# Performance work log

Measured on AMD Instinct MI355X. Metric: run time of the kernel, lower is better.

Reference implementation:

```python
import jax, jax.numpy as jnp
import numpy as np

N_NODES = 50000
N_EDGES = 640000
IN_CH = 64
EDGE_DIM = 16
HID = 128
OUT = 128
L = 5
N_GRAPHS = 128
BN_EPS = 1e-5


def setup_inputs() -> dict:
    key = jax.random.key(0)
    ks = jax.random.split(key, 16)

    def w(k, shape, fan_in):
        return jax.random.normal(k, shape, jnp.float32) / np.sqrt(fan_in)

    inp = {}
    inp["x"] = jax.random.normal(ks[0], (N_NODES, IN_CH), jnp.float32)
    inp["edge_index"] = jax.random.randint(ks[1], (2, N_EDGES), 0, N_NODES)
    inp["edge_attr"] = jax.random.normal(ks[2], (N_EDGES, EDGE_DIM), jnp.float32)
    inp["batch"] = jnp.sort(jax.random.randint(ks[3], (N_NODES,), 0, N_GRAPHS))
    # node / edge encoders
    inp["node_w"] = w(ks[4], (IN_CH, HID), IN_CH)
    inp["node_b"] = jnp.zeros((HID,), jnp.float32)
    inp["edge_w"] = w(ks[5], (EDGE_DIM, HID), EDGE_DIM)
    inp["edge_b"] = jnp.zeros((HID,), jnp.float32)
    # per-layer GINEConv params (stacked over L layers)
    inp["eps"] = jnp.zeros((L,), jnp.float32)  # train_eps init 0
    inp["lin_w"] = w(ks[6], (L, HID, HID), HID)       # GINEConv internal edge lin
    inp["lin_b"] = jnp.zeros((L, HID), jnp.float32)
    inp["mlp1_w"] = w(ks[7], (L, HID, 2 * HID), HID)
    inp["mlp1_b"] = jnp.zeros((L, 2 * HID), jnp.float32)
    inp["mlp2_w"] = w(ks[8], (L, 2 * HID, HID), 2 * HID)
    inp["mlp2_b"] = jnp.zeros((L, HID), jnp.float32)
    inp["bn_g"] = jnp.ones((L, HID), jnp.float32)
    inp["bn_b"] = jnp.zeros((L, HID), jnp.float32)
    # output MLP: HID -> HID//2 -> OUT
    inp["out_w1"] = w(ks[9], (HID, HID // 2), HID)
    inp["out_b1"] = jnp.zeros((HID // 2,), jnp.float32)
    inp["out_w2"] = w(ks[10], (HID // 2, OUT), HID // 2)
    inp["out_b2"] = jnp.zeros((OUT,), jnp.float32)
    return inp


def reference(x, edge_index, edge_attr, batch, node_w, node_b, edge_w, edge_b,
              eps, lin_w, lin_b, mlp1_w, mlp1_b, mlp2_w, mlp2_b, bn_g, bn_b,
              out_w1, out_b1, out_w2, out_b2):
    n_nodes = x.shape[0]
    src, dst = edge_index[0], edge_index[1]
    # node / edge encoders (dropout is identity in eval)
    h = jax.nn.relu(x @ node_w + node_b)            # [N, H]
    e = edge_attr @ edge_w + edge_b                  # [E, H]
    n_layers = lin_w.shape[0]
    for l in range(n_layers):
        # GINEConv: message = relu(x_src + lin(edge_emb)); aggregate = scatter-sum to dst
        m = jax.nn.relu(h[src] + e @ lin_w[l] + lin_b[l])      # [E, H]
        agg = jax.ops.segment_sum(m, dst, num_segments=n_nodes)  # [N, H]
        z = (1.0 + eps[l]) * h + agg
        # GINE MLP: H -> 2H -> H
        z = jax.nn.relu(z @ mlp1_w[l] + mlp1_b[l]) @ mlp2_w[l] + mlp2_b[l]
        # BatchNorm over nodes (training-mode batch statistics)
        mu = z.mean(axis=0)
        var = z.var(axis=0)
        z = (z - mu) * jax.lax.rsqrt(var + BN_EPS) * bn_g[l] + bn_b[l]
        # residual then relu
        h = jax.nn.relu(z + h)
    # global mean pool per graph
    counts = jax.ops.segment_sum(jnp.ones((n_nodes,), h.dtype), batch, num_segments=N_GRAPHS)
    pooled = jax.ops.segment_sum(h, batch, num_segments=N_GRAPHS) / jnp.maximum(counts, 1.0)[:, None]
    # output MLP (dropout identity in eval)
    logits = jax.nn.relu(pooled @ out_w1 + out_b1) @ out_w2 + out_b2
    return (logits, pooled)
```

## Files before the change

### kernel.cpp

```cpp
#include <hip/hip_runtime.h>

#define N_NODES  50000
#define NPAD     50048
#define N_EDGES  640000
#define IN_CH    64
#define EDGE_DIM 16
#define HID      128
#define HID2     256
#define NLAYER   5
#define NGRAPH   128
#define MT64     (NPAD / 64)

typedef unsigned short ushort_t;
typedef __attribute__((ext_vector_type(8))) short short8;
typedef __attribute__((ext_vector_type(4))) short s16x4;
typedef __attribute__((ext_vector_type(4))) float f32x4;
typedef __attribute__((ext_vector_type(2))) float f32x2;

__device__ __forceinline__ float b2f(ushort_t u) {
    union { unsigned v; float f; } x; x.v = ((unsigned)u) << 16; return x.f;
}
__device__ __forceinline__ ushort_t f2b(float f) {
    union { float f; unsigned u; } x; x.f = f;
    unsigned u = x.u;
    unsigned r = (u + 0x7FFFu + ((u >> 16) & 1u)) >> 16;
    return (ushort_t)r;
}

__global__ void k_transpose_cvt(const float* __restrict__ src, ushort_t* __restrict__ dst,
                                int B, int K, int Nn) {
    long total = (long)B * K * Nn;
    for (long i = (long)blockIdx.x * blockDim.x + threadIdx.x; i < total;
         i += (long)gridDim.x * blockDim.x) {
        int b = (int)(i / ((long)K * Nn));
        int rem = (int)(i - (long)b * K * Nn);
        int k = rem / Nn;
        int n = rem - k * Nn;
        dst[(long)b * K * Nn + (long)n * K + k] = f2b(src[i]);
    }
}

__global__ __launch_bounds__(128) void k_combine(const float* __restrict__ ew,
                                                 const float* __restrict__ eb,
                                                 const float* __restrict__ lw,
                                                 const float* __restrict__ lb,
                                                 ushort_t* __restrict__ WcbT,
                                                 float* __restrict__ cc) {
    int l = blockIdx.x, j = threadIdx.x;
    float accW[EDGE_DIM];
#pragma unroll
    for (int k = 0; k < EDGE_DIM; ++k) accW[k] = 0.f;
    float accc = 0.f;
    for (int i = 0; i < HID; ++i) {
        float lwv = lw[((long)l * HID + i) * HID + j];
        accc = fmaf(eb[i], lwv, accc);
#pragma unroll
        for (int k = 0; k < EDGE_DIM; ++k)
            accW[k] = fmaf(ew[k * HID + i], lwv, accW[k]);
    }
    ushort_t* wp = WcbT + ((long)l * HID + j) * 32;
#pragma unroll
    for (int k = 0; k < EDGE_DIM; ++k) wp[k] = f2b(accW[k]);
#pragma unroll
    for (int k = EDGE_DIM; k < 32; ++k) wp[k] = 0;
    cc[l * HID + j] = accc + lb[l * HID + j];
}

__global__ __launch_bounds__(256) void k_hist(const int* __restrict__ ei, int* __restrict__ deg) {
    int e = blockIdx.x * 256 + threadIdx.x;
    if (e < N_EDGES) atomicAdd(&deg[ei[N_EDGES + e]], 1);
}

__global__ __launch_bounds__(1024) void k_scan1(const int* __restrict__ deg,
                                                int* __restrict__ offs, int* __restrict__ bsum) {
    __shared__ int s[1024];
    int i = blockIdx.x * 1024 + threadIdx.x;
    int v = (i < N_NODES) ? deg[i] : 0;
    s[threadIdx.x] = v;
    __syncthreads();
    for (int off = 1; off < 1024; off <<= 1) {
        int t = (threadIdx.x >= off) ? s[threadIdx.x - off] : 0;
        __syncthreads();
        s[threadIdx.x] += t;
        __syncthreads();
    }
    if (i < N_NODES) offs[i] = s[threadIdx.x] - v;
    if (threadIdx.x == 1023) bsum[blockIdx.x] = s[1023];
}

__global__ void k_scan2(int* __restrict__ bsum, int nb) {
    if (threadIdx.x == 0 && blockIdx.x == 0) {
        int acc = 0;
        for (int i = 0; i < nb; ++i) { int v = bsum[i]; bsum[i] = acc; acc += v; }
    }
}

__global__ __launch_bounds__(1024) void k_scan3(int* __restrict__ offs, const int* __restrict__ bsum) {
    int i = blockIdx.x * 1024 + threadIdx.x;
    if (i < N_NODES) offs[i] += bsum[blockIdx.x];
}

__global__ __launch_bounds__(256) void k_scatter(const int* __restrict__ ei,
                                                 const float* __restrict__ ea,
                                                 const int* __restrict__ offs,
                                                 int* __restrict__ cursor,
                                                 int* __restrict__ src_s,
                                                 ushort_t* __restrict__ ea_sb) {
    int e = blockIdx.x * 256 + threadIdx.x;
    if (e >= N_EDGES) return;
    int d = ei[N_EDGES + e];
    int pos = offs[d] + atomicAdd(&cursor[d], 1);
    src_s[pos] = ei[e];
    const f32x4* srcp = (const f32x4*)(ea + (long)e * EDGE_DIM);
    f32x4 v0 = srcp[0], v1 = srcp[1], v2 = srcp[2], v3 = srcp[3];
    short8 o0, o1;
#pragma unroll
    for (int j = 0; j < 4; ++j) {
        o0[j] = (short)f2b(v0[j]); o0[4 + j] = (short)f2b(v1[j]);
        o1[j] = (short)f2b(v2[j]); o1[4 + j] = (short)f2b(v3[j]);
    }
    short8* dst = (short8*)(ea_sb + (long)pos * EDGE_DIM);
    dst[0] = o0;
    dst[1] = o1;
}

__global__ __launch_bounds__(256) void k_node_enc(const float* __restrict__ x,
                                                  const ushort_t* __restrict__ w0T,
                                                  const float* __restrict__ nb,
                                                  float* __restrict__ h,
                                                  ushort_t* __restrict__ hb) {
    __shared__ __align__(16) short lB[HID * IN_CH];
    for (int c = threadIdx.x; c < HID * IN_CH / 8; c += 256) {
        int row = c >> 3, k0 = (c & 7) * 8;
        short8 v = *(const short8*)(w0T + row * IN_CH + k0);
        int g = (k0 >> 3) ^ (row & 7);
        *(short8*)&lB[row * IN_CH + g * 8] = v;
    }
    __syncthreads();
    int wv = threadIdx.x >> 6, l6 = threadIdx.x & 63;
    int lr = l6 & 15, lg = l6 >> 4;
    int grow = blockIdx.x * 64 + wv * 16 + lr;
    f32x4 acc[8];
#pragma unroll
    for (int nt = 0; nt < 8; ++nt) acc[nt] = (f32x4){0.f, 0.f, 0.f, 0.f};
#pragma unroll
    for (int kt = 0; kt < 2; ++kt) {
        int kk = kt * 32 + lg * 8;
        short8 a = {0, 0, 0, 0, 0, 0, 0, 0};
        if (grow < N_NODES) {
            const float* xr = x + (long)grow * IN_CH + kk;
            f32x4 v0 = *(const f32x4*)xr;
            f32x4 v1 = *(const f32x4*)(xr + 4);
#pragma unroll
            for (int j = 0; j < 4; ++j) { a[j] = (short)f2b(v0[j]); a[4 + j] = (short)f2b(v1[j]); }
        }
#pragma unroll
        for (int nt = 0; nt < 8; ++nt) {
            int brow = nt * 16 + lr;
            short8 b = *(const short8*)&lB[brow * IN_CH + (((kk >> 3) ^ (brow & 7)) << 3)];
            acc[nt] = __builtin_amdgcn_mfma_f32_16x16x32_bf16(a, b, acc[nt], 0, 0, 0);
        }
    }
    int orow0 = blockIdx.x * 64 + wv * 16 + lg * 4;
#pragma unroll
    for (int nt = 0; nt < 8; ++nt) {
        int col = nt * 16 + lr;
        float bias = nb[col];
#pragma unroll
        for (int r = 0; r < 4; ++r) {
            int row = orow0 + r;
            if (row < N_NODES) {
                float v = fmaxf(acc[nt][r] + bias, 0.f);
                h[(long)row * HID + col] = v;
                hb[(long)row * HID + col] = f2b(v);
            }
        }
    }
}

__global__ __launch_bounds__(256) void k_edgegemm(const ushort_t* __restrict__ ea_sb,
                                                  const ushort_t* __restrict__ WcbT,
                                                  const float* __restrict__ cc,
                                                  ushort_t* __restrict__ g, int l,
                                                  int ce0, int ce1) {
    int wv = threadIdx.x >> 6, l6 = threadIdx.x & 63;
    int lr = l6 & 15, lg = l6 >> 4;
    short8 af[8];
    f32x4 cv[8];
    const ushort_t* wp = WcbT + (long)l * HID * 32;
#pragma unroll
    for (int nt = 0; nt < 8; ++nt) {
        af[nt] = *(const short8*)(wp + (nt * 16 + lr) * 32 + lg * 8);
        cv[nt] = *(const f32x4*)(cc + l * HID + nt * 16 + lg * 4);
    }
    for (int it = 0; it < 4; ++it) {
        int e0 = ce0 + blockIdx.x * 256 + wv * 64 + it * 16;
        int e = e0 + lr;
        short8 b = {0, 0, 0, 0, 0, 0, 0, 0};
        if (e < ce1 && lg < 2) b = *(const short8*)(ea_sb + (long)e * EDGE_DIM + lg * 8);
        f32x4 acc[8];
#pragma unroll
        for (int nt = 0; nt < 8; ++nt) acc[nt] = (f32x4){0.f, 0.f, 0.f, 0.f};
#pragma unroll
        for (int nt = 0; nt < 8; ++nt)
            acc[nt] = __builtin_amdgcn_mfma_f32_16x16x32_bf16(af[nt], b, acc[nt], 0, 0, 0);
        if (e < ce1) {
            ushort_t* gp = g + (long)(e - ce0) * HID + lg * 4;
#pragma unroll
            for (int nt = 0; nt < 8; ++nt) {
                s16x4 o;
#pragma unroll
                for (int r = 0; r < 4; ++r) o[r] = (short)f2b(acc[nt][r] + cv[nt][r]);
                *(s16x4*)(gp + nt * 16) = o;
            }
        }
    }
}

__global__ __launch_bounds__(256) void k_edge2(const ushort_t* __restrict__ g,
                                               const int* __restrict__ src_s,
                                               const int* __restrict__ offs,
                                               const int* __restrict__ deg,
                                               const float* __restrict__ h,
                                               const ushort_t* __restrict__ hb,
                                               const float* __restrict__ epsv,
                                               float* __restrict__ zacc,
                                               ushort_t* __restrict__ z,
                                               int l, int ce0, int ce1, int mode) {
    int lane = threadIdx.x & 63;
    int node = blockIdx.x * 4 + (threadIdx.x >> 6);
    if (node >= N_NODES) return;
    bool first = mode & 1, last = (mode & 2) != 0;
    int ch0 = lane * 2;
    int s0 = offs[node];
    int dg = deg[node];
    int e_lo = max(s0, ce0);
    int e_hi = min(s0 + dg, ce1);
    if (e_lo >= e_hi && !first && !last) return;
    float a0 = 0.f, a1 = 0.f;
    int i = e_lo;
    for (; i + 4 <= e_hi; i += 4) {
        long eg = (long)(i - ce0);
        int sa = src_s[i], sb_ = src_s[i + 1], sc_ = src_s[i + 2], sd_ = src_s[i + 3];
        unsigned ga = *(const unsigned*)(g + eg * HID + ch0);
        unsigned gb = *(const unsigned*)(g + (eg + 1) * HID + ch0);
        unsigned gc = *(const unsigned*)(g + (eg + 2) * HID + ch0);
        unsigned gd = *(const unsigned*)(g + (eg + 3) * HID + ch0);
        unsigned ha = *(const unsigned*)(hb + (long)sa * HID + ch0);
        unsigned hbv = *(const unsigned*)(hb + (long)sb_ * HID + ch0);
        unsigned hc = *(const unsigned*)(hb + (long)sc_ * HID + ch0);
        unsigned hd = *(const unsigned*)(hb + (long)sd_ * HID + ch0);
        a0 += fmaxf(b2f((ushort_t)(ha & 0xffff)) + b2f((ushort_t)(ga & 0xffff)), 0.f);
        a1 += fmaxf(b2f((ushort_t)(ha >> 16)) + b2f((ushort_t)(ga >> 16)), 0.f);
        a0 += fmaxf(b2f((ushort_t)(hbv & 0xffff)) + b2f((ushort_t)(gb & 0xffff)), 0.f);
        a1 += fmaxf(b2f((ushort_t)(hbv >> 16)) + b2f((ushort_t)(gb >> 16)), 0.f);
        a0 += fmaxf(b2f((ushort_t)(hc & 0xffff)) + b2f((ushort_t)(gc & 0xffff)), 0.f);
        a1 += fmaxf(b2f((ushort_t)(hc >> 16)) + b2f((ushort_t)(gc >> 16)), 0.f);
        a0 += fmaxf(b2f((ushort_t)(hd & 0xffff)) + b2f((ushort_t)(gd & 0xffff)), 0.f);
        a1 += fmaxf(b2f((ushort_t)(hd >> 16)) + b2f((ushort_t)(gd >> 16)), 0.f);
    }
    for (; i < e_hi; ++i) {
        long eg = (long)(i - ce0);
        int s = src_s[i];
        unsigned gv = *(const unsigned*)(g + eg * HID + ch0);
        unsigned hv = *(const unsigned*)(hb + (long)s * HID + ch0);
        a0 += fmaxf(b2f((ushort_t)(hv & 0xffff)) + b2f((ushort_t)(gv & 0xffff)), 0.f);
        a1 += fmaxf(b2f((ushort_t)(hv >> 16)) + b2f((ushort_t)(gv >> 16)), 0.f);
    }
    if (!first) {
        f32x2 p = *(const f32x2*)(zacc + (long)node * HID + ch0);
        a0 += p[0]; a1 += p[1];
    }
    if (last) {
        float ep1 = 1.f + epsv[l];
        f32x2 hn = *(const f32x2*)(h + (long)node * HID + ch0);
        unsigned zz = (unsigned)f2b(fmaf(ep1, hn[0], a0)) |
                      ((unsigned)f2b(fmaf(ep1, hn[1], a1)) << 16);
        *(unsigned*)(z + (long)node * HID + ch0) = zz;
    } else {
        *(f32x2*)(zacc + (long)node * HID + ch0) = (f32x2){a0, a1};
    }
}

__global__ __launch_bounds__(256) void k_mlp1(const ushort_t* __restrict__ z,
                                              const ushort_t* __restrict__ w1T,
                                              const float* __restrict__ b1,
                                              ushort_t* __restrict__ ibuf, int l) {
    __shared__ __align__(16) short lBw[128 * HID];
    __shared__ __align__(16) ushort_t lO[64][136];
    int half = blockIdx.x & 1;
    int mg = blockIdx.x >> 1;
    const ushort_t* wl = w1T + (long)l * HID2 * HID + (long)half * 128 * HID;
    for (int c = threadIdx.x; c < 128 * HID / 8; c += 256) {
        int row = c >> 4, k0 = (c & 15) * 8;
        short8 v = *(const short8*)(wl + row * HID + k0);
        int gsw = (k0 >> 3) ^ (row & 7);
        *(short8*)&lBw[row * HID + gsw * 8] = v;
    }
    __syncthreads();
    int wv = threadIdx.x >> 6, l6 = threadIdx.x & 63;
    int lr = l6 & 15, lg = l6 >> 4;
    float bv[8];
#pragma unroll
    for (int nt = 0; nt < 8; ++nt) bv[nt] = b1[l * HID2 + half * 128 + nt * 16 + lr];
    for (int tile = mg; tile < MT64; tile += 512) {
        const ushort_t* zr = z + (long)(tile * 64 + wv * 16 + lr) * HID;
        short8 a[4];
#pragma unroll
        for (int kt = 0; kt < 4; ++kt) a[kt] = *(const short8*)(zr + kt * 32 + lg * 8);
        f32x4 acc[8];
#pragma unroll
        for (int nt = 0; nt < 8; ++nt) acc[nt] = (f32x4){0.f, 0.f, 0.f, 0.f};
#pragma unroll
        for (int kt = 0; kt < 4; ++kt) {
#pragma unroll
            for (int nt = 0; nt < 8; ++nt) {
                int brow = nt * 16 + lr;
                short8 b = *(const short8*)&lBw[brow * HID + (((kt * 4 + lg) ^ (brow & 7)) << 3)];
                acc[nt] = __builtin_amdgcn_mfma_f32_16x16x32_bf16(a[kt], b, acc[nt], 0, 0, 0);
            }
        }
#pragma unroll
        for (int nt = 0; nt < 8; ++nt) {
#pragma unroll
            for (int r = 0; r < 4; ++r)
                lO[wv * 16 + lg * 4 + r][nt * 16 + lr] = f2b(fmaxf(acc[nt][r] + bv[nt], 0.f));
        }
        __syncthreads();
        for (int c = threadIdx.x; c < 64 * 128 / 8; c += 256) {
            int row = c >> 4, c8 = (c & 15) * 8;
            *(short8*)(ibuf + (long)(tile * 64 + row) * HID2 + half * 128 + c8) =
                *(const short8*)&lO[row][c8];
        }
        __syncthreads();
    }
}

__global__ __launch_bounds__(256) void k_mlp2(const ushort_t* __restrict__ ibuf,
                                              const ushort_t* __restrict__ w2T,
                                              const float* __restrict__ b2,
                                              ushort_t* __restrict__ z2,
                                              float* __restrict__ bnstats, int l) {
    __shared__ __align__(16) short lBw[64 * HID2];
    __shared__ __align__(16) ushort_t lO[64][72];
    int half = blockIdx.x & 1;
    int mg = blockIdx.x >> 1;
    const ushort_t* wl = w2T + (long)l * HID * HID2 + (long)half * 64 * HID2;
    for (int c = threadIdx.x; c < 64 * HID2 / 8; c += 256) {
        int row = c >> 5, k0 = (c & 31) * 8;
        short8 v = *(const short8*)(wl + row * HID2 + k0);
        int gsw = (k0 >> 3) ^ (row & 7);
        *(short8*)&lBw[row * HID2 + gsw * 8] = v;
    }
    __syncthreads();
    int wv = threadIdx.x >> 6, l6 = threadIdx.x & 63;
    int lr = l6 & 15, lg = l6 >> 4;
    float bv[4];
#pragma unroll
    for (int nt = 0; nt < 4; ++nt) bv[nt] = b2[l * HID + half * 64 + nt * 16 + lr];
    float bS[4] = {0.f, 0.f, 0.f, 0.f}, bQ[4] = {0.f, 0.f, 0.f, 0.f};
    for (int tile = mg; tile < MT64; tile += 512) {
        const ushort_t* ir = ibuf + (long)(tile * 64 + wv * 16 + lr) * HID2;
        short8 a[8];
#pragma unroll
        for (int kt = 0; kt < 8; ++kt) a[kt] = *(const short8*)(ir + kt * 32 + lg * 8);
        f32x4 acc[4];
#pragma unroll
        for (int nt = 0; nt < 4; ++nt) acc[nt] = (f32x4){0.f, 0.f, 0.f, 0.f};
#pragma unroll
        for (int kt = 0; kt < 8; ++kt) {
#pragma unroll
            for (int nt = 0; nt < 4; ++nt) {
                int brow = nt * 16 + lr;
                short8 b = *(const short8*)&lBw[brow * HID2 + (((kt * 4 + lg) ^ (brow & 7)) << 3)];
                acc[nt] = __builtin_amdgcn_mfma_f32_16x16x32_bf16(a[kt], b, acc[nt], 0, 0, 0);
            }
        }
        int rbase = tile * 64 + wv * 16 + lg * 4;
#pragma unroll
        for (int nt = 0; nt < 4; ++nt) {
#pragma unroll
            for (int r = 0; r < 4; ++r) {
                float v = acc[nt][r] + bv[nt];
                lO[wv * 16 + lg * 4 + r][nt * 16 + lr] = f2b(v);
                if (rbase + r < N_NODES) { bS[nt] += v; bQ[nt] += v * v; }
            }
        }
        __syncthreads();
        for (int c = threadIdx.x; c < 64 * 64 / 8; c += 256) {
            int row = c >> 3, c8 = (c & 7) * 8;
            *(short8*)(z2 + (long)(tile * 64 + row) * HID + half * 64 + c8) =
                *(const short8*)&lO[row][c8];
        }
        __syncthreads();
    }
#pragma unroll
    for (int nt = 0; nt < 4; ++nt) {
        float s = bS[nt], q = bQ[nt];
        s += __shfl_xor(s, 16); s += __shfl_xor(s, 32);
        q += __shfl_xor(q, 16); q += __shfl_xor(q, 32);
        if (lg == 0) {
            int col = half * 64 + nt * 16 + lr;
            atomicAdd(&bnstats[l * HID + col], s);
            atomicAdd(&bnstats[(NLAYER + l) * HID + col], q);
        }
    }
}

__global__ __launch_bounds__(1024) void k_resid(const ushort_t* __restrict__ z2,
                                                const float* __restrict__ bnstats,
                                                const float* __restrict__ bng,
                                                const float* __restrict__ bnb,
                                                float* __restrict__ h,
                                                ushort_t* __restrict__ hb, int l) {
    long i = (long)blockIdx.x * 1024 + threadIdx.x;
    int c = (int)(i & (HID - 1));
    float inv = 1.f / (float)N_NODES;
    float mu = bnstats[l * HID + c] * inv;
    float var = bnstats[(NLAYER + l) * HID + c] * inv - mu * mu;
    float A = rsqrtf(var + 1e-5f) * bng[l * HID + c];
    float B = bnb[l * HID + c] - mu * A;
    float v = fmaf(b2f(z2[i]), A, B) + h[i];
    v = fmaxf(v, 0.f);
    h[i] = v;
    hb[i] = f2b(v);
}

__global__ void k_gstart(const int* __restrict__ batch, int* __restrict__ gstart) {
    int g = threadIdx.x;
    if (g > NGRAPH) return;
    int lo = 0, hi = N_NODES;
    while (lo < hi) { int mid = (lo + hi) >> 1; if (batch[mid] < g) lo = mid + 1; else hi = mid; }
    gstart[g] = lo;
}

__global__ __launch_bounds__(512) void k_pool(const float* __restrict__ h,
                                              const int* __restrict__ gstart,
                                              float* __restrict__ pooled,
                                              float* __restrict__ outp) {
    __shared__ float red[4][HID];
    int g = blockIdx.x;
    int ch = threadIdx.x & 127, seg = threadIdx.x >> 7;
    int st = gstart[g], en = gstart[g + 1];
    float s = 0.f;
    for (int i = st + seg; i < en; i += 4) s += h[(long)i * HID + ch];
    red[seg][ch] = s;
    __syncthreads();
    if (seg == 0) {
        float p = (red[0][ch] + red[1][ch] + red[2][ch] + red[3][ch]) /
                  fmaxf((float)(en - st), 1.f);
        pooled[g * HID + ch] = p;
        outp[g * HID + ch] = p;
    }
}

__global__ __launch_bounds__(128) void k_outmlp(const float* __restrict__ pooled,
                                                const float* __restrict__ w1,
                                                const float* __restrict__ b1,
                                                const float* __restrict__ w2,
                                                const float* __restrict__ b2,
                                                float* __restrict__ outl) {
    __shared__ float pr[HID];
    __shared__ float hid[64];
    int g = blockIdx.x, t = threadIdx.x;
    pr[t] = pooled[g * HID + t];
    __syncthreads();
    if (t < 64) {
        float a = b1[t];
        for (int k = 0; k < HID; ++k) a = fmaf(pr[k], w1[k * 64 + t], a);
        hid[t] = fmaxf(a, 0.f);
    }
    __syncthreads();
    float a = b2[t];
#pragma unroll
    for (int j = 0; j < 64; ++j) a = fmaf(hid[j], w2[j * HID + t], a);
    outl[g * HID + t] = a;
}

extern "C" void kernel_launch(void* const* d_in, const int* in_sizes, int n_in,
                              void* d_out, int out_size, void* d_ws, size_t ws_size,
                              hipStream_t stream) {
    (void)in_sizes; (void)n_in; (void)out_size;
    const float* x      = (const float*)d_in[0];
    const int*   ei     = (const int*)d_in[1];
    const float* ea     = (const float*)d_in[2];
    const int*   batch  = (const int*)d_in[3];
    const float* node_w = (const float*)d_in[4];
    const float* node_b = (const float*)d_in[5];
    const float* edge_w = (const float*)d_in[6];
    const float* edge_b = (const float*)d_in[7];
    const float* epsv   = (const float*)d_in[8];
    const float* lin_w  = (const float*)d_in[9];
    const float* lin_b  = (const float*)d_in[10];
    const float* m1w    = (const float*)d_in[11];
    const float* m1b    = (const float*)d_in[12];
    const float* m2w    = (const float*)d_in[13];
    const float* m2b    = (const float*)d_in[14];
    const float* bng    = (const float*)d_in[15];
    const float* bnb    = (const float*)d_in[16];
    const float* ow1    = (const float*)d_in[17];
    const float* ob1    = (const float*)d_in[18];
    const float* ow2    = (const float*)d_in[19];
    const float* ob2    = (const float*)d_in[20];

    const size_t MiB = 1024ull * 1024ull;
    int NC;
    if      (ws_size >= 275 * MiB) NC = 1;
    else if (ws_size >= 193 * MiB) NC = 2;
    else if (ws_size >= 152 * MiB) NC = 4;
    else                           NC = 8;
    int EC = (N_EDGES + NC - 1) / NC;

    char* ws = (char*)d_ws;
    size_t off = 0;
    auto alloc = [&](size_t bytes) -> char* {
        char* p = ws + off;
        off = (off + bytes + 255) & ~(size_t)255;
        return p;
    };
    float*    h       = (float*)alloc((size_t)NPAD * HID * 4);
    ushort_t* hb      = (ushort_t*)alloc((size_t)NPAD * HID * 2);
    ushort_t* z       = (ushort_t*)alloc((size_t)NPAD * HID * 2);
    ushort_t* ibuf    = (ushort_t*)alloc((size_t)NPAD * HID2 * 2);
    ushort_t* ea_sb   = (ushort_t*)alloc((size_t)N_EDGES * EDGE_DIM * 2 + 64);
    ushort_t* g       = (ushort_t*)alloc((size_t)EC * HID * 2);
    int*      src_s   = (int*)alloc((size_t)N_EDGES * 4);
    int*      deg     = (int*)alloc((size_t)N_NODES * 4);
    int*      offs    = (int*)alloc((size_t)N_NODES * 4);
    int*      cursor  = (int*)alloc((size_t)N_NODES * 4);
    int*      bsum    = (int*)alloc(64 * 4);
    ushort_t* WcbT    = (ushort_t*)alloc((size_t)NLAYER * HID * 32 * 2);
    float*    cc      = (float*)alloc((size_t)NLAYER * HID * 4);
    ushort_t* w0T     = (ushort_t*)alloc((size_t)HID * IN_CH * 2);
    ushort_t* w1T     = (ushort_t*)alloc((size_t)NLAYER * HID2 * HID * 2);
    ushort_t* w2T     = (ushort_t*)alloc((size_t)NLAYER * HID * HID2 * 2);
    float*    bnstats = (float*)alloc((size_t)2 * NLAYER * HID * 4);
    int*      gstart  = (int*)alloc((NGRAPH + 1) * 4);
    float*    pooled  = (float*)alloc((size_t)NGRAPH * HID * 4);
    float*    zacc    = (float*)ibuf;
    ushort_t* z2      = z;

    (void)hipMemsetAsync(deg, 0, (size_t)N_NODES * 4, stream);
    (void)hipMemsetAsync(cursor, 0, (size_t)N_NODES * 4, stream);
    (void)hipMemsetAsync(bnstats, 0, (size_t)2 * NLAYER * HID * 4, stream);

    k_transpose_cvt<<<64, 256, 0, stream>>>(node_w, w0T, 1, IN_CH, HID);
    k_transpose_cvt<<<640, 256, 0, stream>>>(m1w, w1T, NLAYER, HID, HID2);
    k_transpose_cvt<<<640, 256, 0, stream>>>(m2w, w2T, NLAYER, HID2, HID);
    k_combine<<<NLAYER, HID, 0, stream>>>(edge_w, edge_b, lin_w, lin_b, WcbT, cc);

    k_hist<<<N_EDGES / 256, 256, 0, stream>>>(ei, deg);
    k_scan1<<<49, 1024, 0, stream>>>(deg, offs, bsum);
    k_scan2<<<1, 1, 0, stream>>>(bsum, 49);
    k_scan3<<<49, 1024, 0, stream>>>(offs, bsum);
    k_scatter<<<N_EDGES / 256, 256, 0, stream>>>(ei, ea, offs, cursor, src_s, ea_sb);

    k_node_enc<<<NPAD / 64, 256, 0, stream>>>(x, w0T, node_b, h, hb);

    for (int l = 0; l < NLAYER; ++l) {
        for (int c = 0; c < NC; ++c) {
            int ce0 = c * EC;
            int ce1 = (ce0 + EC < N_EDGES) ? (ce0 + EC) : N_EDGES;
            int nblk = (ce1 - ce0 + 255) / 256;
            int mode = (c == 0 ? 1 : 0) | (c == NC - 1 ? 2 : 0);
            k_edgegemm<<<nblk, 256, 0, stream>>>(ea_sb, WcbT, cc, g, l, ce0, ce1);
            k_edge2<<<(N_NODES + 3) / 4, 256, 0, stream>>>(g, src_s, offs, deg, h, hb,
                                                           epsv, zacc, z, l, ce0, ce1, mode);
        }
        k_mlp1<<<1024, 256, 0, stream>>>(z, w1T, m1b, ibuf, l);
        k_mlp2<<<1024, 256, 0, stream>>>(ibuf, w2T, m2b, z2, bnstats, l);
        k_resid<<<(N_NODES * HID) / 1024, 1024, 0, stream>>>(z2, bnstats, bng, bnb, h, hb, l);
    }

    k_gstart<<<1, 256, 0, stream>>>(batch, gstart);
    k_pool<<<NGRAPH, 512, 0, stream>>>(h, gstart, pooled, (float*)d_out + NGRAPH * HID);
    k_outmlp<<<NGRAPH, HID, 0, stream>>>(pooled, ow1, ob1, ow2, ob2, (float*)d_out);
}
```

Before: 1.182 ms.

## Transpose MFMA operands in MLP kernels, store directly, prefetch next tile

Swaps MFMA operand roles in both MLP kernels so each lane's accumulator holds four consecutive output channels of one node. Lanes then write bf16 results straight to global memory, with no LDS staging buffer and no two __syncthreads per tile. The next tile's activations are loaded into registers while the current tile computes. The cost is narrower 8-byte global stores and more registers for the prefetch buffers and the per-row BN statistics, which now need a deeper shuffle reduction.

```diff
diff --git a/kernel.cpp b/kernel.cpp
--- a/kernel.cpp
+++ b/kernel.cpp
@@ -287,7 +287,6 @@
                                               const float* __restrict__ b1,
                                               ushort_t* __restrict__ ibuf, int l) {
     __shared__ __align__(16) short lBw[128 * HID];
-    __shared__ __align__(16) ushort_t lO[64][136];
     int half = blockIdx.x & 1;
     int mg = blockIdx.x >> 1;
     const ushort_t* wl = w1T + (long)l * HID2 * HID + (long)half * 128 * HID;
@@ -300,39 +299,43 @@
     __syncthreads();
     int wv = threadIdx.x >> 6, l6 = threadIdx.x & 63;
     int lr = l6 & 15, lg = l6 >> 4;
-    float bv[8];
-#pragma unroll
-    for (int nt = 0; nt < 8; ++nt) bv[nt] = b1[l * HID2 + half * 128 + nt * 16 + lr];
-    for (int tile = mg; tile < MT64; tile += 512) {
+    f32x4 bv[8];
+#pragma unroll
+    for (int nt = 0; nt < 8; ++nt)
+        bv[nt] = *(const f32x4*)(b1 + l * HID2 + half * 128 + nt * 16 + lg * 4);
+    int tile = mg;
+    short8 b[4];
+    {
         const ushort_t* zr = z + (long)(tile * 64 + wv * 16 + lr) * HID;
-        short8 a[4];
-#pragma unroll
-        for (int kt = 0; kt < 4; ++kt) a[kt] = *(const short8*)(zr + kt * 32 + lg * 8);
-        f32x4 acc[8];
-#pragma unroll
-        for (int nt = 0; nt < 8; ++nt) acc[nt] = (f32x4){0.f, 0.f, 0.f, 0.f};
-#pragma unroll
-        for (int kt = 0; kt < 4; ++kt) {
-#pragma unroll
-            for (int nt = 0; nt < 8; ++nt) {
-                int brow = nt * 16 + lr;
-                short8 b = *(const short8*)&lBw[brow * HID + (((kt * 4 + lg) ^ (brow & 7)) << 3)];
-                acc[nt] = __builtin_amdgcn_mfma_f32_16x16x32_bf16(a[kt], b, acc[nt], 0, 0, 0);
+#pragma unroll
+        for (int kt = 0; kt < 4; ++kt) b[kt] = *(const short8*)(zr + kt * 32 + lg * 8);
+    }
+    while (tile < MT64) {
+        int ntile = tile + 512;
+        short8 bn_[4];
+        if (ntile < MT64) {
+            const ushort_t* zr = z + (long)(ntile * 64 + wv * 16 + lr) * HID;
+#pragma unroll
+            for (int kt = 0; kt < 4; ++kt) bn_[kt] = *(const short8*)(zr + kt * 32 + lg * 8);
+        }
+        int node = tile * 64 + wv * 16 + lr;
+#pragma unroll
+        for (int nt = 0; nt < 8; ++nt) {
+            f32x4 acc = (f32x4){0.f, 0.f, 0.f, 0.f};
+            int brow = nt * 16 + lr;
+#pragma unroll
+            for (int kt = 0; kt < 4; ++kt) {
+                short8 af = *(const short8*)&lBw[brow * HID + (((kt * 4 + lg) ^ (brow & 7)) << 3)];
+                acc = __builtin_amdgcn_mfma_f32_16x16x32_bf16(af, b[kt], acc, 0, 0, 0);
             }
-        }
-#pragma unroll
-        for (int nt = 0; nt < 8; ++nt) {
-#pragma unroll
-            for (int r = 0; r < 4; ++r)
-                lO[wv * 16 + lg * 4 + r][nt * 16 + lr] = f2b(fmaxf(acc[nt][r] + bv[nt], 0.f));
-        }
-        __syncthreads();
-        for (int c = threadIdx.x; c < 64 * 128 / 8; c += 256) {
-            int row = c >> 4, c8 = (c & 15) * 8;
-            *(short8*)(ibuf + (long)(tile * 64 + row) * HID2 + half * 128 + c8) =
-                *(const short8*)&lO[row][c8];
-        }
-        __syncthreads();
+            s16x4 o;
+#pragma unroll
+            for (int r = 0; r < 4; ++r) o[r] = (short)f2b(fmaxf(acc[r] + bv[nt][r], 0.f));
+            *(s16x4*)(ibuf + (long)node * HID2 + half * 128 + nt * 16 + lg * 4) = o;
+        }
+        tile = ntile;
+#pragma unroll
+        for (int kt = 0; kt < 4; ++kt) b[kt] = bn_[kt];
     }
 }
 
@@ -342,7 +345,6 @@
                                               ushort_t* __restrict__ z2,
                                               float* __restrict__ bnstats, int l) {
     __shared__ __align__(16) short lBw[64 * HID2];
-    __shared__ __align__(16) ushort_t lO[64][72];
     int half = blockIdx.x & 1;
     int mg = blockIdx.x >> 1;
     const ushort_t* wl = w2T + (long)l * HID * HID2 + (long)half * 64 * HID2;
@@ -355,54 +357,68 @@
     __syncthreads();
     int wv = threadIdx.x >> 6, l6 = threadIdx.x & 63;
     int lr = l6 & 15, lg = l6 >> 4;
-    float bv[4];
-#pragma unroll
-    for (int nt = 0; nt < 4; ++nt) bv[nt] = b2[l * HID + half * 64 + nt * 16 + lr];
-    float bS[4] = {0.f, 0.f, 0.f, 0.f}, bQ[4] = {0.f, 0.f, 0.f, 0.f};
-    for (int tile = mg; tile < MT64; tile += 512) {
+    f32x4 bv[4];
+#pragma unroll
+    for (int nt = 0; nt < 4; ++nt)
+        bv[nt] = *(const f32x4*)(b2 + l * HID + half * 64 + nt * 16 + lg * 4);
+    float bS[4][4], bQ[4][4];
+#pragma unroll
+    for (int nt = 0; nt < 4; ++nt)
+#pragma unroll
+        for (int r = 0; r < 4; ++r) { bS[nt][r] = 0.f; bQ[nt][r] = 0.f; }
+    int tile = mg;
+    short8 b[8];
+    {
         const ushort_t* ir = ibuf + (long)(tile * 64 + wv * 16 + lr) * HID2;
-        short8 a[8];
-#pragma unroll
-        for (int kt = 0; kt < 8; ++kt) a[kt] = *(const short8*)(ir + kt * 32 + lg * 8);
-        f32x4 acc[4];
-#pragma unroll
-        for (int nt = 0; nt < 4; ++nt) acc[nt] = (f32x4){0.f, 0.f, 0.f, 0.f};
-#pragma unroll
-        for (int kt = 0; kt < 8; ++kt) {
-#pragma unroll
-            for (int nt = 0; nt < 4; ++nt) {
-                int brow = nt * 16 + lr;
-                short8 b = *(const short8*)&lBw[brow * HID2 + (((kt * 4 + lg) ^ (brow & 7)) << 3)];
-                acc[nt] = __builtin_amdgcn_mfma_f32_16x16x32_bf16(a[kt], b, acc[nt], 0, 0, 0);
+#pragma unroll
+        for (int kt = 0; kt < 8; ++kt) b[kt] = *(const short8*)(ir + kt * 32 + lg * 8);
+    }
+    while (tile < MT64) {
+        int ntile = tile + 512;
+        short8 bn_[8];
+        if (ntile < MT64) {
+            const ushort_t* ir = ibuf + (long)(ntile * 64 + wv * 16 + lr) * HID2;
+#pragma unroll
+            for (int kt = 0; kt < 8; ++kt) bn_[kt] = *(const short8*)(ir + kt * 32 + lg * 8);
+        }
+        int node = tile * 64 + wv * 16 + lr;
+        bool valid = node < N_NODES;
+#pragma unroll
+        for (int nt = 0; nt < 4; ++nt) {
+            f32x4 acc = (f32x4){0.f, 0.f, 0.f, 0.f};
+            int brow = nt * 16 + lr;
+#pragma unroll
+            for (int kt = 0; kt < 8; ++kt) {
+                short8 af = *(const short8*)&lBw[brow * HID2 + (((kt * 4 + lg) ^ (brow & 7)) << 3)];
+                acc = __builtin_amdgcn_mfma_f32_16x16x32_bf16(af, b[kt], acc, 0, 0, 0);
             }
-        }
-        int rbase = tile * 64 + wv * 16 + lg * 4;
-#pragma unroll
-        for (int nt = 0; nt < 4; ++nt) {
+            s16x4 o;
 #pragma unroll
             for (int r = 0; r < 4; ++r) {
-                float v = acc[nt][r] + bv[nt];
-                lO[wv * 16 + lg * 4 + r][nt * 16 + lr] = f2b(v);
-                if (rbase + r < N_NODES) { bS[nt] += v; bQ[nt] += v * v; }
+                float v = acc[r] + bv[nt][r];
+                o[r] = (short)f2b(v);
+                if (valid) { bS[nt][r] += v; bQ[nt][r] += v * v; }
             }
-        }
-        __syncthreads();
-        for (int c = threadIdx.x; c < 64 * 64 / 8; c += 256) {
-            int row = c >> 3, c8 = (c & 7) * 8;
-            *(short8*)(z2 + (long)(tile * 64 + row) * HID + half * 64 + c8) =
-                *(const short8*)&lO[row][c8];
-        }
-        __syncthreads();
+            *(s16x4*)(z2 + (long)node * HID + half * 64 + nt * 16 + lg * 4) = o;
+        }
+        tile = ntile;
+#pragma unroll
+        for (int kt = 0; kt < 8; ++kt) b[kt] = bn_[kt];
     }
 #pragma unroll
     for (int nt = 0; nt < 4; ++nt) {
-        float s = bS[nt], q = bQ[nt];
-        s += __shfl_xor(s, 16); s += __shfl_xor(s, 32);
-        q += __shfl_xor(q, 16); q += __shfl_xor(q, 32);
-        if (lg == 0) {
-            int col = half * 64 + nt * 16 + lr;
-            atomicAdd(&bnstats[l * HID + col], s);
-            atomicAdd(&bnstats[(NLAYER + l) * HID + col], q);
+#pragma unroll
+        for (int r = 0; r < 4; ++r) {
+            float s = bS[nt][r], q = bQ[nt][r];
+            s += __shfl_xor(s, 1); s += __shfl_xor(s, 2);
+            s += __shfl_xor(s, 4); s += __shfl_xor(s, 8);
+            q += __shfl_xor(q, 1); q += __shfl_xor(q, 2);
+            q += __shfl_xor(q, 4); q += __shfl_xor(q, 8);
+            if (lr == 0) {
+                int col = half * 64 + nt * 16 + lg * 4 + r;
+                atomicAdd(&bnstats[l * HID + col], s);
+                atomicAdd(&bnstats[(NLAYER + l) * HID + col], q);
+            }
         }
     }
 }
```

Result: slower. 2.031 ms (+71.9%).
